# Kernel tuning notes

Hardware: AMD Instinct MI355X
Metric: run time of the kernel (lower is better)

## Reference

```python
import jax, jax.numpy as jnp
import numpy as np

T, SEQ, IN, H, L, NC = 64, 128, 256, 512, 2, 10


def _xavier(key, shape):
    fan_out, fan_in = shape[0], shape[1]
    a = jnp.sqrt(6.0 / (fan_in + fan_out)).astype(jnp.float32)
    return jax.random.uniform(key, shape, jnp.float32, -a, a)


def setup_inputs() -> dict:
    key = jax.random.key(0)
    ks = jax.random.split(key, 16)
    inp = {"x": jax.random.normal(ks[0], (T, SEQ, IN), jnp.float32)}
    # LSTM layer 0 (input IN), layer 1 (input H). PyTorch gate order: i, f, g, o
    inp["w_ih0"] = _xavier(ks[1], (4 * H, IN))
    inp["w_hh0"] = _xavier(ks[2], (4 * H, H))
    inp["b_ih0"] = jnp.zeros((4 * H,), jnp.float32)
    inp["b_hh0"] = jnp.zeros((4 * H,), jnp.float32)
    inp["w_ih1"] = _xavier(ks[3], (4 * H, H))
    inp["w_hh1"] = _xavier(ks[4], (4 * H, H))
    inp["b_ih1"] = jnp.zeros((4 * H,), jnp.float32)
    inp["b_hh1"] = jnp.zeros((4 * H,), jnp.float32)
    # out_linear: Linear(SEQ*H, H) -> ReLU -> Linear(H, NC)
    inp["w1"] = _xavier(ks[5], (H, SEQ * H))
    inp["b1"] = jnp.zeros((H,), jnp.float32)
    inp["w2"] = _xavier(ks[6], (NC, H))
    inp["b2"] = jnp.zeros((NC,), jnp.float32)
    return inp


def _lstm_layer(x, w_ih, w_hh, b_ih, b_hh):
    # x: [T, B, I]; returns hidden sequence [T, B, H]
    B = x.shape[1]
    Hh = w_hh.shape[1]
    # precompute input-to-gate contributions for all timesteps
    xg = jnp.einsum('tbi,gi->tbg', x, w_ih) + b_ih  # [T, B, 4H]

    def step(carry, xg_t):
        h, c = carry
        g = xg_t + h @ w_hh.T + b_hh  # [B, 4H]
        i, f, gg, o = jnp.split(g, 4, axis=-1)
        i = jax.nn.sigmoid(i)
        f = jax.nn.sigmoid(f)
        gg = jnp.tanh(gg)
        o = jax.nn.sigmoid(o)
        c = f * c + i * gg
        h = o * jnp.tanh(c)
        return (h, c), h

    init = (jnp.zeros((B, Hh), x.dtype), jnp.zeros((B, Hh), x.dtype))
    _, ys = jax.lax.scan(step, init, xg)
    return ys


def reference(x, w_ih0, w_hh0, b_ih0, b_hh0, w_ih1, w_hh1, b_ih1, b_hh1, w1, b1, w2, b2):
    out = _lstm_layer(x, w_ih0, w_hh0, b_ih0, b_hh0)
    out = _lstm_layer(out, w_ih1, w_hh1, b_ih1, b_hh1)  # [T, SEQ, H]
    # dropout p=0.0 -> identity
    flat = out.reshape(out.shape[0], -1)  # [T, SEQ*H] (batched version of per-i loop)
    hmid = jax.nn.relu(flat @ w1.T + b1)
    return hmid @ w2.T + b2  # [T, NC]
```

## Files before the change

### kernel.cpp

```cpp
#include <hip/hip_runtime.h>

#define TT 64
#define BB 128
#define IND 256
#define HH 512
#define GG 2048
#define NCC 10
#define KFLAT 65536
#define HP2 520
#define SP 36

typedef __attribute__((ext_vector_type(8))) short bf16x8;
typedef __attribute__((ext_vector_type(4))) float floatx4;

__device__ __forceinline__ unsigned short f2bf(float x) {
    unsigned u = __builtin_bit_cast(unsigned, x);
    u += 0x7fffu + ((u >> 16) & 1u);
    return (unsigned short)(u >> 16);
}
__device__ __forceinline__ float bf2f(unsigned short h) {
    unsigned u = ((unsigned)h) << 16;
    return __builtin_bit_cast(float, u);
}
__device__ __forceinline__ float pk2f(unsigned u) {
    float hi = __builtin_bit_cast(float, u & 0xffff0000u);
    float lo = __builtin_bit_cast(float, u << 16);
    return hi + lo;
}

__global__ __launch_bounds__(256) void pack_split_kernel(
    const float* __restrict__ src, unsigned* __restrict__ dst, int n)
{
    for (int i = blockIdx.x * 256 + threadIdx.x; i < n; i += gridDim.x * 256) {
        float f = src[i];
        unsigned short hb = f2bf(f);
        unsigned short lb = f2bf(f - bf2f(hb));
        dst[i] = ((unsigned)hb << 16) | lb;
    }
}

__global__ __launch_bounds__(256) void gemm_pk_mfma(
    const unsigned* __restrict__ A, const unsigned* __restrict__ W,
    const float* __restrict__ b0, const float* __restrict__ b1,
    float* __restrict__ C, int K, int N)
{
    __shared__ short Ahi[128][SP], Alo[128][SP], Whi[128][SP], Wlo[128][SP];

    const int tid  = threadIdx.x;
    const int lane = tid & 63;
    const int wv   = tid >> 6;
    const int wm   = (wv & 1) * 64;
    const int wn   = (wv >> 1) * 64;
    const int l15  = lane & 15;
    const int quad = lane >> 4;
    const int m0   = blockIdx.x * 128;
    const int n0   = blockIdx.y * 128;

    floatx4 acc[4][4];
    #pragma unroll
    for (int i = 0; i < 4; ++i)
        #pragma unroll
        for (int j = 0; j < 4; ++j)
            acc[i][j] = (floatx4){0.f, 0.f, 0.f, 0.f};

    for (int kc = 0; kc < K; kc += 32) {
        #pragma unroll
        for (int it = 0; it < 4; ++it) {
            const int lin = it * 256 + tid;
            const int row = lin >> 3;
            const int c4  = (lin & 7) * 4;
            uint4 va = *(const uint4*)&A[(size_t)(m0 + row) * K + kc + c4];
            uint2 ah, al;
            ah.x = (va.x >> 16) | (va.y & 0xffff0000u);
            ah.y = (va.z >> 16) | (va.w & 0xffff0000u);
            al.x = (va.x & 0xffffu) | (va.y << 16);
            al.y = (va.z & 0xffffu) | (va.w << 16);
            *(uint2*)&Ahi[row][c4] = ah;
            *(uint2*)&Alo[row][c4] = al;
            uint4 vw = *(const uint4*)&W[(size_t)(n0 + row) * K + kc + c4];
            uint2 wh, wl;
            wh.x = (vw.x >> 16) | (vw.y & 0xffff0000u);
            wh.y = (vw.z >> 16) | (vw.w & 0xffff0000u);
            wl.x = (vw.x & 0xffffu) | (vw.y << 16);
            wl.y = (vw.z & 0xffffu) | (vw.w << 16);
            *(uint2*)&Whi[row][c4] = wh;
            *(uint2*)&Wlo[row][c4] = wl;
        }
        __syncthreads();

        bf16x8 afh[4], afl[4], bfh[4], bfl[4];
        #pragma unroll
        for (int i = 0; i < 4; ++i) {
            afh[i] = *(const bf16x8*)&Ahi[wm + i * 16 + l15][quad * 8];
            afl[i] = *(const bf16x8*)&Alo[wm + i * 16 + l15][quad * 8];
            bfh[i] = *(const bf16x8*)&Whi[wn + i * 16 + l15][quad * 8];
            bfl[i] = *(const bf16x8*)&Wlo[wn + i * 16 + l15][quad * 8];
        }
        #pragma unroll
        for (int i = 0; i < 4; ++i)
            #pragma unroll
            for (int j = 0; j < 4; ++j) {
                acc[i][j] = __builtin_amdgcn_mfma_f32_16x16x32_bf16(afh[i], bfh[j], acc[i][j], 0, 0, 0);
                acc[i][j] = __builtin_amdgcn_mfma_f32_16x16x32_bf16(afh[i], bfl[j], acc[i][j], 0, 0, 0);
                acc[i][j] = __builtin_amdgcn_mfma_f32_16x16x32_bf16(afl[i], bfh[j], acc[i][j], 0, 0, 0);
            }
        __syncthreads();
    }

    #pragma unroll
    for (int i = 0; i < 4; ++i) {
        #pragma unroll
        for (int j = 0; j < 4; ++j) {
            const int n = n0 + wn + j * 16 + l15;
            const float bias = b0[n] + b1[n];
            #pragma unroll
            for (int r = 0; r < 4; ++r) {
                const int m = m0 + wm + i * 16 + quad * 4 + r;
                C[(size_t)m * N + n] = acc[i][j][r] + bias;
            }
        }
    }
}

__device__ __forceinline__ unsigned stage8_atomic(
    const unsigned long long* __restrict__ src, int bb, int kk, unsigned exp,
    short (*Hs_hi)[HP2], short (*Hs_lo)[HP2])
{
    unsigned long long q0 = __hip_atomic_load(src + 0, __ATOMIC_RELAXED, __HIP_MEMORY_SCOPE_AGENT);
    unsigned long long q1 = __hip_atomic_load(src + 1, __ATOMIC_RELAXED, __HIP_MEMORY_SCOPE_AGENT);
    unsigned long long q2 = __hip_atomic_load(src + 2, __ATOMIC_RELAXED, __HIP_MEMORY_SCOPE_AGENT);
    unsigned long long q3 = __hip_atomic_load(src + 3, __ATOMIC_RELAXED, __HIP_MEMORY_SCOPE_AGENT);
    unsigned c0 = (unsigned)q0, c1 = (unsigned)(q0 >> 32);
    unsigned c2 = (unsigned)q1, c3 = (unsigned)(q1 >> 32);
    unsigned c4 = (unsigned)q2, c5 = (unsigned)(q2 >> 32);
    unsigned c6 = (unsigned)q3, c7 = (unsigned)(q3 >> 32);
    unsigned bad = ((c0 ^ exp) | (c1 ^ exp) | (c2 ^ exp) | (c3 ^ exp)
                  | (c4 ^ exp) | (c5 ^ exp) | (c6 ^ exp) | (c7 ^ exp)) & 0xFu;
    uint4 hiv, lov;
    hiv.x = (c0 >> 16) | (c1 & 0xffff0000u);
    hiv.y = (c2 >> 16) | (c3 & 0xffff0000u);
    hiv.z = (c4 >> 16) | (c5 & 0xffff0000u);
    hiv.w = (c6 >> 16) | (c7 & 0xffff0000u);
    lov.x = (c0 & 0xFFF0u) | ((c1 & 0xFFF0u) << 16);
    lov.y = (c2 & 0xFFF0u) | ((c3 & 0xFFF0u) << 16);
    lov.z = (c4 & 0xFFF0u) | ((c5 & 0xFFF0u) << 16);
    lov.w = (c6 & 0xFFF0u) | ((c7 & 0xFFF0u) << 16);
    *(uint4*)&Hs_hi[bb][kk] = hiv;
    *(uint4*)&Hs_lo[bb][kk] = lov;
    return bad;
}

__device__ __forceinline__ unsigned stage8_plain(
    const unsigned* __restrict__ src, int bb, int kk, unsigned exp,
    short (*Hs_hi)[HP2], short (*Hs_lo)[HP2])
{
    const uint4 v0 = *(const uint4*)(src);
    const uint4 v1 = *(const uint4*)(src + 4);
    unsigned bad = ((v0.x ^ exp) | (v0.y ^ exp) | (v0.z ^ exp) | (v0.w ^ exp)
                  | (v1.x ^ exp) | (v1.y ^ exp) | (v1.z ^ exp) | (v1.w ^ exp)) & 0xFu;
    uint4 hiv, lov;
    hiv.x = (v0.x >> 16) | (v0.y & 0xffff0000u);
    hiv.y = (v0.z >> 16) | (v0.w & 0xffff0000u);
    hiv.z = (v1.x >> 16) | (v1.y & 0xffff0000u);
    hiv.w = (v1.z >> 16) | (v1.w & 0xffff0000u);
    lov.x = (v0.x & 0xFFF0u) | ((v0.y & 0xFFF0u) << 16);
    lov.y = (v0.z & 0xFFF0u) | ((v0.w & 0xFFF0u) << 16);
    lov.z = (v1.x & 0xFFF0u) | ((v1.y & 0xFFF0u) << 16);
    lov.w = (v1.z & 0xFFF0u) | ((v1.w & 0xFFF0u) << 16);
    *(uint4*)&Hs_hi[bb][kk] = hiv;
    *(uint4*)&Hs_lo[bb][kk] = lov;
    return bad;
}

__device__ __forceinline__ void stage_tile_g(
    const unsigned* __restrict__ base, unsigned exp,
    int tstart, int pcount, int pstride,
    short (*Hs_hi)[HP2], short (*Hs_lo)[HP2])
{
    unsigned miss = 0;
    for (int p = 0; p < pcount; ++p) {
        const int idx = p * pstride + tstart;
        unsigned bad = stage8_plain(base + idx, idx >> 9, idx & 511,
                                    exp, Hs_hi, Hs_lo);
        miss |= (bad ? 1u : 0u) << p;
    }
    while (miss) {
        for (int p = 0; p < pcount; ++p) {
            if (miss & (1u << p)) {
                const int idx = p * pstride + tstart;
                if (!stage8_atomic((const unsigned long long*)(base + idx),
                                   idx >> 9, idx & 511, exp, Hs_hi, Hs_lo))
                    miss &= ~(1u << p);
            }
        }
    }
}

__device__ __forceinline__ void spin_flag(const unsigned* p) {
    int n = 0;
    while (__hip_atomic_load(p, __ATOMIC_RELAXED, __HIP_MEMORY_SCOPE_AGENT) == 0u) {
        if (++n > 65536) break;
    }
}

__global__ __launch_bounds__(512, 2) void lstm_fused(
    const float* __restrict__ xg,
    const float* __restrict__ w_hh0,
    const float* __restrict__ w_ih1,
    const float* __restrict__ w_hh1,
    const float* __restrict__ b_ih1, const float* __restrict__ b_hh1,
    unsigned* __restrict__ hpack0,
    unsigned* __restrict__ hpack1,
    unsigned* __restrict__ flags)
{
    __shared__ short Ra_hi[32][HP2], Ra_lo[32][HP2];
    __shared__ short Xa_hi[32][HP2], Xa_lo[32][HP2];
    __shared__ float GsR[64][33];
    __shared__ float GsX[64][33];

    const int tid  = threadIdx.x;
    const int lane = tid & 63;
    const int wv   = tid >> 6;
    const bool isR = wv < 4;
    const int gate = wv & 3;
    const bool isB = blockIdx.x >= 128;
    const int blk  = blockIdx.x & 127;
    const int bt   = blk & 3;
    const int jsl  = blk >> 2;
    const int j0   = jsl * 16;
    const int l15  = lane & 15;
    const int quad = lane >> 4;
    const int tid_x = tid - 256;

    bf16x8 wf_hi[16], wf_lo[16];
    {
        const float* wsrc = isR ? (isB ? w_hh1 : w_hh0) : w_ih1;
        if (isR || isB) {
            const float* wrow = wsrc + (size_t)(gate * HH + j0 + l15) * HH + quad * 8;
            #pragma unroll
            for (int kc = 0; kc < 16; ++kc) {
                float f[8];
                *(float4*)&f[0] = *(const float4*)&wrow[kc * 32];
                *(float4*)&f[4] = *(const float4*)&wrow[kc * 32 + 4];
                bf16x8 vh, vl;
                #pragma unroll
                for (int j = 0; j < 8; ++j) {
                    unsigned short hb = f2bf(f[j]);
                    vh[j] = (short)hb;
                    vl[j] = (short)f2bf(f[j] - bf2f(hb));
                }
                wf_hi[kc] = vh; wf_lo[kc] = vl;
            }
        }
    }

    const int j_u = tid & 15;
    const int bu  = (tid >> 4) & 15;
    float bias_i = 0.f, bias_f = 0.f, bias_g = 0.f, bias_o = 0.f;
    if (isB && isR) {
        bias_i = b_ih1[j0 + j_u]            + b_hh1[j0 + j_u];
        bias_f = b_ih1[HH + j0 + j_u]       + b_hh1[HH + j0 + j_u];
        bias_g = b_ih1[2 * HH + j0 + j_u]   + b_hh1[2 * HH + j0 + j_u];
        bias_o = b_ih1[3 * HH + j0 + j_u]   + b_hh1[3 * HH + j0 + j_u];
    }

    for (int i = tid; i < 64 * 33; i += 512)
        ((float*)GsX)[i] = 0.f;
    __syncthreads();

    unsigned* hp_rec = isB ? hpack1 : hpack0;
    const int layerBase = isB ? 65 : 0;
    float c0 = 0.f, c1 = 0.f;

    for (int t = 0; t < TT; ++t) {
        const unsigned* rec_base = hp_rec + (size_t)t * (BB * HH) + (size_t)bt * 32 * HH;
        const unsigned* inp_base = hpack0 + (size_t)(t + 1) * (BB * HH) + (size_t)bt * 32 * HH;
        const unsigned expR = (unsigned)t % 9u;
        const unsigned expX = (unsigned)(t + 1) % 9u;
        const unsigned* fR = flags + ((layerBase + t) * 4 + bt) * 32;
        const unsigned* fX = flags + ((t + 1) * 4 + bt) * 32;

        float xgv[2][4];
        if (!isB && isR) {
            #pragma unroll
            for (int ccell = 0; ccell < 2; ++ccell) {
                const int b = bu + ccell * 16;
                const float* base = xg + (size_t)t * (BB * GG)
                                  + (size_t)(bt * 32 + b) * GG + j0 + j_u;
                xgv[ccell][0] = base[0];
                xgv[ccell][1] = base[HH];
                xgv[ccell][2] = base[2 * HH];
                xgv[ccell][3] = base[3 * HH];
            }
        }

        if (wv == 0 && lane < 32 && t > 0 && lane != jsl) spin_flag(fR + lane);
        if (isB && wv == 4 && lane < 32) spin_flag(fX + lane);
        __syncthreads();

        if (isB) {
            if (isR) stage_tile_g(rec_base, expR, tid * 8,   8, 2048, Ra_hi, Ra_lo);
            else     stage_tile_g(inp_base, expX, tid_x * 8, 8, 2048, Xa_hi, Xa_lo);
        } else {
            stage_tile_g(rec_base, expR, tid * 8, 4, 4096, Ra_hi, Ra_lo);
        }
        __syncthreads();

        if (isR) {
            floatx4 a0 = {0.f,0.f,0.f,0.f}, a1 = {0.f,0.f,0.f,0.f};
            #pragma unroll
            for (int kc = 0; kc < 16; ++kc) {
                const int off = kc * 32 + quad * 8;
                bf16x8 r0h = *(const bf16x8*)&Ra_hi[l15][off];
                bf16x8 r0l = *(const bf16x8*)&Ra_lo[l15][off];
                bf16x8 r1h = *(const bf16x8*)&Ra_hi[16 + l15][off];
                bf16x8 r1l = *(const bf16x8*)&Ra_lo[16 + l15][off];
                a0 = __builtin_amdgcn_mfma_f32_16x16x32_bf16(wf_hi[kc], r0h, a0, 0, 0, 0);
                a1 = __builtin_amdgcn_mfma_f32_16x16x32_bf16(wf_hi[kc], r1h, a1, 0, 0, 0);
                a0 = __builtin_amdgcn_mfma_f32_16x16x32_bf16(wf_hi[kc], r0l, a0, 0, 0, 0);
                a1 = __builtin_amdgcn_mfma_f32_16x16x32_bf16(wf_hi[kc], r1l, a1, 0, 0, 0);
                a0 = __builtin_amdgcn_mfma_f32_16x16x32_bf16(wf_lo[kc], r0h, a0, 0, 0, 0);
                a1 = __builtin_amdgcn_mfma_f32_16x16x32_bf16(wf_lo[kc], r1h, a1, 0, 0, 0);
            }
            #pragma unroll
            for (int r = 0; r < 4; ++r) {
                GsR[gate * 16 + quad * 4 + r][l15]      = a0[r];
                GsR[gate * 16 + quad * 4 + r][16 + l15] = a1[r];
            }
        } else if (isB) {
            floatx4 a0 = {0.f,0.f,0.f,0.f}, a1 = {0.f,0.f,0.f,0.f};
            #pragma unroll
            for (int kc = 0; kc < 16; ++kc) {
                const int off = kc * 32 + quad * 8;
                bf16x8 x0h = *(const bf16x8*)&Xa_hi[l15][off];
                bf16x8 x0l = *(const bf16x8*)&Xa_lo[l15][off];
                bf16x8 x1h = *(const bf16x8*)&Xa_hi[16 + l15][off];
                bf16x8 x1l = *(const bf16x8*)&Xa_lo[16 + l15][off];
                a0 = __builtin_amdgcn_mfma_f32_16x16x32_bf16(wf_hi[kc], x0h, a0, 0, 0, 0);
                a1 = __builtin_amdgcn_mfma_f32_16x16x32_bf16(wf_hi[kc], x1h, a1, 0, 0, 0);
                a0 = __builtin_amdgcn_mfma_f32_16x16x32_bf16(wf_hi[kc], x0l, a0, 0, 0, 0);
                a1 = __builtin_amdgcn_mfma_f32_16x16x32_bf16(wf_hi[kc], x1l, a1, 0, 0, 0);
                a0 = __builtin_amdgcn_mfma_f32_16x16x32_bf16(wf_lo[kc], x0h, a0, 0, 0, 0);
                a1 = __builtin_amdgcn_mfma_f32_16x16x32_bf16(wf_lo[kc], x1h, a1, 0, 0, 0);
            }
            #pragma unroll
            for (int r = 0; r < 4; ++r) {
                GsX[gate * 16 + quad * 4 + r][l15]      = a0[r];
                GsX[gate * 16 + quad * 4 + r][16 + l15] = a1[r];
            }
        }
        __syncthreads();

        if (isR) {
            const unsigned tag = (unsigned)(t + 1) % 9u;
            #pragma unroll
            for (int ccell = 0; ccell < 2; ++ccell) {
                const int b = bu + ccell * 16;
                float gi = GsR[j_u][b]      + GsX[j_u][b];
                float gf = GsR[16 + j_u][b] + GsX[16 + j_u][b];
                float gg = GsR[32 + j_u][b] + GsX[32 + j_u][b];
                float go = GsR[48 + j_u][b] + GsX[48 + j_u][b];
                if (isB) { gi += bias_i; gf += bias_f; gg += bias_g; go += bias_o; }
                else     { gi += xgv[ccell][0]; gf += xgv[ccell][1];
                           gg += xgv[ccell][2]; go += xgv[ccell][3]; }
                const float si = 1.f / (1.f + __expf(-gi));
                const float sf = 1.f / (1.f + __expf(-gf));
                const float tg = 2.f / (1.f + __expf(-2.f * gg)) - 1.f;
                const float so = 1.f / (1.f + __expf(-go));
                float& cr = ccell ? c1 : c0;
                cr = sf * cr + si * tg;
                const float th = 2.f / (1.f + __expf(-2.f * cr)) - 1.f;
                const float hval = so * th;
                const unsigned short hb = f2bf(hval);
                const unsigned short lb = f2bf(hval - bf2f(hb));
                const unsigned pk = ((unsigned)hb << 16) | ((unsigned)lb & 0xFFF0u) | tag;
                __hip_atomic_store(
                    &hp_rec[(size_t)(t + 1) * (BB * HH) + (size_t)(bt * 32 + b) * HH + j0 + j_u],
                    pk, __ATOMIC_RELAXED, __HIP_MEMORY_SCOPE_AGENT);
            }
        }
        __syncthreads();

        if (tid == 0)
            __hip_atomic_store(
                flags + ((layerBase + (t + 1)) * 4 + bt) * 32 + jsl,
                1u, __ATOMIC_RELAXED, __HIP_MEMORY_SCOPE_AGENT);
    }
}

__global__ __launch_bounds__(256) void cls_partial_kernel(
    const unsigned* __restrict__ A, const float* __restrict__ W,
    float* __restrict__ part)
{
    const int n0 = blockIdx.x * 64;
    const int s  = blockIdx.y;
    const int kbase = s * 2048;
    const int tid = threadIdx.x;
    __shared__ float As[32][68];
    __shared__ float Bs[32][68];
    const int tm = tid >> 4, tn = tid & 15;
    float acc[4][4] = {};

    for (int kt = 0; kt < 2048; kt += 32) {
        #pragma unroll
        for (int q = tid; q < 512; q += 256) {
            const int mm = q >> 3;
            const int kq = q & 7;
            uint4 v = *(const uint4*)&A[(size_t)mm * KFLAT + kbase + kt + kq * 4];
            As[kq*4+0][mm] = pk2f(v.x & 0xFFFFFFF0u); As[kq*4+1][mm] = pk2f(v.y & 0xFFFFFFF0u);
            As[kq*4+2][mm] = pk2f(v.z & 0xFFFFFFF0u); As[kq*4+3][mm] = pk2f(v.w & 0xFFFFFFF0u);
            float4 w = *(const float4*)&W[(size_t)(n0 + mm) * KFLAT + kbase + kt + kq * 4];
            Bs[kq*4+0][mm] = w.x; Bs[kq*4+1][mm] = w.y;
            Bs[kq*4+2][mm] = w.z; Bs[kq*4+3][mm] = w.w;
        }
        __syncthreads();
        #pragma unroll
        for (int k = 0; k < 32; ++k) {
            float4 a = *(const float4*)&As[k][tm * 4];
            float4 b = *(const float4*)&Bs[k][tn * 4];
            acc[0][0] += a.x*b.x; acc[0][1] += a.x*b.y; acc[0][2] += a.x*b.z; acc[0][3] += a.x*b.w;
            acc[1][0] += a.y*b.x; acc[1][1] += a.y*b.y; acc[1][2] += a.y*b.z; acc[1][3] += a.y*b.w;
            acc[2][0] += a.z*b.x; acc[2][1] += a.z*b.y; acc[2][2] += a.z*b.z; acc[2][3] += a.z*b.w;
            acc[3][0] += a.w*b.x; acc[3][1] += a.w*b.y; acc[3][2] += a.w*b.z; acc[3][3] += a.w*b.w;
        }
        __syncthreads();
    }
    #pragma unroll
    for (int i = 0; i < 4; ++i) {
        const int m = tm * 4 + i;
        #pragma unroll
        for (int j = 0; j < 4; ++j) {
            part[((size_t)s * 64 + m) * 512 + n0 + tn * 4 + j] = acc[i][j];
        }
    }
}

__global__ __launch_bounds__(256) void cls_final_kernel(
    const float* __restrict__ part, const float* __restrict__ b1,
    const float* __restrict__ w2, const float* __restrict__ b2,
    float* __restrict__ out)
{
    const int t = blockIdx.x;
    __shared__ float hm[512];
    for (int n = threadIdx.x; n < 512; n += 256) {
        float sacc = b1[n];
        for (int sl = 0; sl < 32; ++sl)
            sacc += part[((size_t)sl * 64 + t) * 512 + n];
        hm[n] = fmaxf(sacc, 0.f);
    }
    __syncthreads();
    if (threadIdx.x < NCC) {
        float sacc = b2[threadIdx.x];
        const float* wr = w2 + (size_t)threadIdx.x * 512;
        for (int n = 0; n < 512; ++n) sacc += hm[n] * wr[n];
        out[t * NCC + threadIdx.x] = sacc;
    }
}

extern "C" void kernel_launch(void* const* d_in, const int* in_sizes, int n_in,
                              void* d_out, int out_size, void* d_ws, size_t ws_size,
                              hipStream_t stream)
{
    const float* x     = (const float*)d_in[0];
    const float* w_ih0 = (const float*)d_in[1];
    const float* w_hh0 = (const float*)d_in[2];
    const float* b_ih0 = (const float*)d_in[3];
    const float* b_hh0 = (const float*)d_in[4];
    const float* w_ih1 = (const float*)d_in[5];
    const float* w_hh1 = (const float*)d_in[6];
    const float* b_ih1 = (const float*)d_in[7];
    const float* b_hh1 = (const float*)d_in[8];
    const float* w1    = (const float*)d_in[9];
    const float* b1    = (const float*)d_in[10];
    const float* w2    = (const float*)d_in[11];
    const float* b2    = (const float*)d_in[12];
    float* out = (float*)d_out;

    float*    ws     = (float*)d_ws;
    float*    xg     = ws;
    unsigned* hpack0 = (unsigned*)(xg + (size_t)8192 * 2048);
    unsigned* hpack1 = hpack0 + (size_t)65 * BB * HH;
    unsigned* xpk    = hpack1;
    unsigned* w0pk   = xpk + (size_t)8192 * IND;
    float*    part   = (float*)(hpack1 + (size_t)65 * BB * HH);
    unsigned* flags  = (unsigned*)part;

    pack_split_kernel<<<1024, 256, 0, stream>>>(x, xpk, 8192 * IND);
    pack_split_kernel<<<512,  256, 0, stream>>>(w_ih0, w0pk, GG * IND);
    hipMemsetAsync(hpack0, 0, (size_t)BB * HH * sizeof(unsigned), stream);
    hipMemsetAsync(flags, 0, (size_t)2 * 65 * 4 * 32 * sizeof(unsigned), stream);

    gemm_pk_mfma<<<dim3(8192 / 128, GG / 128), 256, 0, stream>>>(
        xpk, w0pk, b_ih0, b_hh0, xg, IND, GG);

    hipMemsetAsync(hpack1, 0, (size_t)BB * HH * sizeof(unsigned), stream);

    lstm_fused<<<256, 512, 0, stream>>>(
        xg, w_hh0, w_ih1, w_hh1, b_ih1, b_hh1, hpack0, hpack1, flags);

    cls_partial_kernel<<<dim3(512 / 64, 32), 256, 0, stream>>>(
        hpack1 + (size_t)BB * HH, w1, part);
    cls_final_kernel<<<64, 256, 0, stream>>>(part, b1, w2, b2, out);
}
```

Before: 818.5 us.

## Replace flag barriers with per-wave counters and distributed spin-waits in fused LSTM

Each of the four gate waves now does its own fetch-add on the per-block flag after its hidden-state stores drain, replacing the block-wide barrier plus a single flag write from thread 0. Consumers spin per lane until the counter reaches four, with s_sleep backoff, and two block-wide __syncthreads per timestep are removed. The epilogue is remapped so each thread handles two adjacent hidden units for one batch row, using float2 loads for xg and 64-bit packed atomic stores. The aim is to cut barrier latency on the recurrent critical path. In exchange, the lighter ordering between the counters and the LDS staging may be fragile, and a correctness risk remains if counters are not reset between launches.

```diff
diff --git a/kernel.cpp b/kernel.cpp
--- a/kernel.cpp
+++ b/kernel.cpp
@@ -196,9 +196,10 @@
     }
 }
 
-__device__ __forceinline__ void spin_flag(const unsigned* p) {
+__device__ __forceinline__ void spin_cnt(const unsigned* p) {
     int n = 0;
-    while (__hip_atomic_load(p, __ATOMIC_RELAXED, __HIP_MEMORY_SCOPE_AGENT) == 0u) {
+    while (__hip_atomic_load(p, __ATOMIC_RELAXED, __HIP_MEMORY_SCOPE_AGENT) < 4u) {
+        __builtin_amdgcn_s_sleep(1);
         if (++n > 65536) break;
     }
 }
@@ -231,6 +232,7 @@
     const int l15  = lane & 15;
     const int quad = lane >> 4;
     const int tid_x = tid - 256;
+    const int slice = (lane >> 1);
 
     bf16x8 wf_hi[16], wf_lo[16];
     {
@@ -254,14 +256,18 @@
         }
     }
 
-    const int j_u = tid & 15;
-    const int bu  = (tid >> 4) & 15;
-    float bias_i = 0.f, bias_f = 0.f, bias_g = 0.f, bias_o = 0.f;
+    const int ju  = (tid & 7) * 2;
+    const int bu2 = (tid >> 3) & 31;
+    float bi0=0.f,bi1=0.f,bf0_=0.f,bf1_=0.f,bg0=0.f,bg1=0.f,bo0=0.f,bo1=0.f;
     if (isB && isR) {
-        bias_i = b_ih1[j0 + j_u]            + b_hh1[j0 + j_u];
-        bias_f = b_ih1[HH + j0 + j_u]       + b_hh1[HH + j0 + j_u];
-        bias_g = b_ih1[2 * HH + j0 + j_u]   + b_hh1[2 * HH + j0 + j_u];
-        bias_o = b_ih1[3 * HH + j0 + j_u]   + b_hh1[3 * HH + j0 + j_u];
+        bi0 = b_ih1[j0+ju]        + b_hh1[j0+ju];
+        bi1 = b_ih1[j0+ju+1]      + b_hh1[j0+ju+1];
+        bf0_= b_ih1[HH+j0+ju]     + b_hh1[HH+j0+ju];
+        bf1_= b_ih1[HH+j0+ju+1]   + b_hh1[HH+j0+ju+1];
+        bg0 = b_ih1[2*HH+j0+ju]   + b_hh1[2*HH+j0+ju];
+        bg1 = b_ih1[2*HH+j0+ju+1] + b_hh1[2*HH+j0+ju+1];
+        bo0 = b_ih1[3*HH+j0+ju]   + b_hh1[3*HH+j0+ju];
+        bo1 = b_ih1[3*HH+j0+ju+1] + b_hh1[3*HH+j0+ju+1];
     }
 
     for (int i = tid; i < 64 * 33; i += 512)
@@ -277,26 +283,25 @@
         const unsigned* inp_base = hpack0 + (size_t)(t + 1) * (BB * HH) + (size_t)bt * 32 * HH;
         const unsigned expR = (unsigned)t % 9u;
         const unsigned expX = (unsigned)(t + 1) % 9u;
-        const unsigned* fR = flags + ((layerBase + t) * 4 + bt) * 32;
-        const unsigned* fX = flags + ((t + 1) * 4 + bt) * 32;
-
-        float xgv[2][4];
+        const unsigned* cR = flags + ((layerBase + t) * 4 + bt) * 32;
+        const unsigned* cX = flags + ((t + 1) * 4 + bt) * 32;
+
+        float2 xgv[4];
         if (!isB && isR) {
-            #pragma unroll
-            for (int ccell = 0; ccell < 2; ++ccell) {
-                const int b = bu + ccell * 16;
-                const float* base = xg + (size_t)t * (BB * GG)
-                                  + (size_t)(bt * 32 + b) * GG + j0 + j_u;
-                xgv[ccell][0] = base[0];
-                xgv[ccell][1] = base[HH];
-                xgv[ccell][2] = base[2 * HH];
-                xgv[ccell][3] = base[3 * HH];
-            }
-        }
-
-        if (wv == 0 && lane < 32 && t > 0 && lane != jsl) spin_flag(fR + lane);
-        if (isB && wv == 4 && lane < 32) spin_flag(fX + lane);
-        __syncthreads();
+            const float* base = xg + (size_t)t * (BB * GG)
+                              + (size_t)(bt * 32 + bu2) * GG + j0 + ju;
+            #pragma unroll
+            for (int g = 0; g < 4; ++g)
+                xgv[g] = *(const float2*)&base[g * HH];
+        }
+
+        if (isB) {
+            if (isR) { if (t > 0) spin_cnt(cR + slice); }
+            else     { spin_cnt(cX + slice); }
+        } else {
+            if (t > 0) spin_cnt(cR + slice);
+        }
+        asm volatile("" ::: "memory");
 
         if (isB) {
             if (isR) stage_tile_g(rec_base, expR, tid * 8,   8, 2048, Ra_hi, Ra_lo);
@@ -353,38 +358,56 @@
 
         if (isR) {
             const unsigned tag = (unsigned)(t + 1) % 9u;
-            #pragma unroll
-            for (int ccell = 0; ccell < 2; ++ccell) {
-                const int b = bu + ccell * 16;
-                float gi = GsR[j_u][b]      + GsX[j_u][b];
-                float gf = GsR[16 + j_u][b] + GsX[16 + j_u][b];
-                float gg = GsR[32 + j_u][b] + GsX[32 + j_u][b];
-                float go = GsR[48 + j_u][b] + GsX[48 + j_u][b];
-                if (isB) { gi += bias_i; gf += bias_f; gg += bias_g; go += bias_o; }
-                else     { gi += xgv[ccell][0]; gf += xgv[ccell][1];
-                           gg += xgv[ccell][2]; go += xgv[ccell][3]; }
-                const float si = 1.f / (1.f + __expf(-gi));
-                const float sf = 1.f / (1.f + __expf(-gf));
-                const float tg = 2.f / (1.f + __expf(-2.f * gg)) - 1.f;
-                const float so = 1.f / (1.f + __expf(-go));
-                float& cr = ccell ? c1 : c0;
-                cr = sf * cr + si * tg;
-                const float th = 2.f / (1.f + __expf(-2.f * cr)) - 1.f;
-                const float hval = so * th;
-                const unsigned short hb = f2bf(hval);
-                const unsigned short lb = f2bf(hval - bf2f(hb));
-                const unsigned pk = ((unsigned)hb << 16) | ((unsigned)lb & 0xFFF0u) | tag;
-                __hip_atomic_store(
-                    &hp_rec[(size_t)(t + 1) * (BB * HH) + (size_t)(bt * 32 + b) * HH + j0 + j_u],
-                    pk, __ATOMIC_RELAXED, __HIP_MEMORY_SCOPE_AGENT);
-            }
-        }
-        __syncthreads();
-
-        if (tid == 0)
+            float gi0 = GsR[ju][bu2]      + GsX[ju][bu2];
+            float gi1 = GsR[ju+1][bu2]    + GsX[ju+1][bu2];
+            float gf0 = GsR[16+ju][bu2]   + GsX[16+ju][bu2];
+            float gf1 = GsR[17+ju][bu2]   + GsX[17+ju][bu2];
+            float gg0 = GsR[32+ju][bu2]   + GsX[32+ju][bu2];
+            float gg1 = GsR[33+ju][bu2]   + GsX[33+ju][bu2];
+            float go0 = GsR[48+ju][bu2]   + GsX[48+ju][bu2];
+            float go1 = GsR[49+ju][bu2]   + GsX[49+ju][bu2];
+            if (isB) {
+                gi0 += bi0; gi1 += bi1; gf0 += bf0_; gf1 += bf1_;
+                gg0 += bg0; gg1 += bg1; go0 += bo0; go1 += bo1;
+            } else {
+                gi0 += xgv[0].x; gi1 += xgv[0].y;
+                gf0 += xgv[1].x; gf1 += xgv[1].y;
+                gg0 += xgv[2].x; gg1 += xgv[2].y;
+                go0 += xgv[3].x; go1 += xgv[3].y;
+            }
+            const float si0 = 1.f / (1.f + __expf(-gi0));
+            const float sf0 = 1.f / (1.f + __expf(-gf0));
+            const float tg0 = 2.f / (1.f + __expf(-2.f * gg0)) - 1.f;
+            const float so0 = 1.f / (1.f + __expf(-go0));
+            c0 = sf0 * c0 + si0 * tg0;
+            const float th0 = 2.f / (1.f + __expf(-2.f * c0)) - 1.f;
+            const float h0v = so0 * th0;
+            const float si1 = 1.f / (1.f + __expf(-gi1));
+            const float sf1 = 1.f / (1.f + __expf(-gf1));
+            const float tg1 = 2.f / (1.f + __expf(-2.f * gg1)) - 1.f;
+            const float so1 = 1.f / (1.f + __expf(-go1));
+            c1 = sf1 * c1 + si1 * tg1;
+            const float th1 = 2.f / (1.f + __expf(-2.f * c1)) - 1.f;
+            const float h1v = so1 * th1;
+            const unsigned short hb0 = f2bf(h0v);
+            const unsigned short lb0 = f2bf(h0v - bf2f(hb0));
+            const unsigned short hb1 = f2bf(h1v);
+            const unsigned short lb1 = f2bf(h1v - bf2f(hb1));
+            const unsigned pk0 = ((unsigned)hb0 << 16) | ((unsigned)lb0 & 0xFFF0u) | tag;
+            const unsigned pk1 = ((unsigned)hb1 << 16) | ((unsigned)lb1 & 0xFFF0u) | tag;
+            const unsigned long long pk64 =
+                (unsigned long long)pk0 | ((unsigned long long)pk1 << 32);
             __hip_atomic_store(
-                flags + ((layerBase + (t + 1)) * 4 + bt) * 32 + jsl,
-                1u, __ATOMIC_RELAXED, __HIP_MEMORY_SCOPE_AGENT);
+                (unsigned long long*)&hp_rec[(size_t)(t + 1) * (BB * HH)
+                    + (size_t)(bt * 32 + bu2) * HH + j0 + ju],
+                pk64, __ATOMIC_RELAXED, __HIP_MEMORY_SCOPE_AGENT);
+
+            asm volatile("s_waitcnt vmcnt(0)" ::: "memory");
+            if (lane == 0)
+                __hip_atomic_fetch_add(
+                    (unsigned*)(flags + ((layerBase + (t + 1)) * 4 + bt) * 32 + jsl),
+                    1u, __ATOMIC_RELAXED, __HIP_MEMORY_SCOPE_AGENT);
+        }
     }
 }
 
```

Result: slower. 1.193 ms (+45.8%).

## Fuse layer-0 input projection into persistent LSTM kernel, drop xg GEMM

Applied to the files above, without the earlier changes.

Removes the separate pack kernels and the large input-projection GEMM that wrote a 64x128x2048 fp32 xg buffer. Layer-0 blocks now use their previously idle X-waves to load w_ih0 fragments into registers once, convert x[t] to split bf16 in LDS each step, and compute the input gate contributions with MFMA alongside the recurrent part. This cuts a kernel launch and the xg write and re-read. In exchange, the per-step critical path of layer 0 gains the x conversion and an extra MFMA loop, and layer-0 R-waves now stage the full tile rather than half.

```diff
diff --git a/kernel.cpp b/kernel.cpp
--- a/kernel.cpp
+++ b/kernel.cpp
@@ -8,7 +8,6 @@
 #define NCC 10
 #define KFLAT 65536
 #define HP2 520
-#define SP 36
 
 typedef __attribute__((ext_vector_type(8))) short bf16x8;
 typedef __attribute__((ext_vector_type(4))) float floatx4;
@@ -26,100 +25,6 @@
     float hi = __builtin_bit_cast(float, u & 0xffff0000u);
     float lo = __builtin_bit_cast(float, u << 16);
     return hi + lo;
-}
-
-__global__ __launch_bounds__(256) void pack_split_kernel(
-    const float* __restrict__ src, unsigned* __restrict__ dst, int n)
-{
-    for (int i = blockIdx.x * 256 + threadIdx.x; i < n; i += gridDim.x * 256) {
-        float f = src[i];
-        unsigned short hb = f2bf(f);
-        unsigned short lb = f2bf(f - bf2f(hb));
-        dst[i] = ((unsigned)hb << 16) | lb;
-    }
-}
-
-__global__ __launch_bounds__(256) void gemm_pk_mfma(
-    const unsigned* __restrict__ A, const unsigned* __restrict__ W,
-    const float* __restrict__ b0, const float* __restrict__ b1,
-    float* __restrict__ C, int K, int N)
-{
-    __shared__ short Ahi[128][SP], Alo[128][SP], Whi[128][SP], Wlo[128][SP];
-
-    const int tid  = threadIdx.x;
-    const int lane = tid & 63;
-    const int wv   = tid >> 6;
-    const int wm   = (wv & 1) * 64;
-    const int wn   = (wv >> 1) * 64;
-    const int l15  = lane & 15;
-    const int quad = lane >> 4;
-    const int m0   = blockIdx.x * 128;
-    const int n0   = blockIdx.y * 128;
-
-    floatx4 acc[4][4];
-    #pragma unroll
-    for (int i = 0; i < 4; ++i)
-        #pragma unroll
-        for (int j = 0; j < 4; ++j)
-            acc[i][j] = (floatx4){0.f, 0.f, 0.f, 0.f};
-
-    for (int kc = 0; kc < K; kc += 32) {
-        #pragma unroll
-        for (int it = 0; it < 4; ++it) {
-            const int lin = it * 256 + tid;
-            const int row = lin >> 3;
-            const int c4  = (lin & 7) * 4;
-            uint4 va = *(const uint4*)&A[(size_t)(m0 + row) * K + kc + c4];
-            uint2 ah, al;
-            ah.x = (va.x >> 16) | (va.y & 0xffff0000u);
-            ah.y = (va.z >> 16) | (va.w & 0xffff0000u);
-            al.x = (va.x & 0xffffu) | (va.y << 16);
-            al.y = (va.z & 0xffffu) | (va.w << 16);
-            *(uint2*)&Ahi[row][c4] = ah;
-            *(uint2*)&Alo[row][c4] = al;
-            uint4 vw = *(const uint4*)&W[(size_t)(n0 + row) * K + kc + c4];
-            uint2 wh, wl;
-            wh.x = (vw.x >> 16) | (vw.y & 0xffff0000u);
-            wh.y = (vw.z >> 16) | (vw.w & 0xffff0000u);
-            wl.x = (vw.x & 0xffffu) | (vw.y << 16);
-            wl.y = (vw.z & 0xffffu) | (vw.w << 16);
-            *(uint2*)&Whi[row][c4] = wh;
-            *(uint2*)&Wlo[row][c4] = wl;
-        }
-        __syncthreads();
-
-        bf16x8 afh[4], afl[4], bfh[4], bfl[4];
-        #pragma unroll
-        for (int i = 0; i < 4; ++i) {
-            afh[i] = *(const bf16x8*)&Ahi[wm + i * 16 + l15][quad * 8];
-            afl[i] = *(const bf16x8*)&Alo[wm + i * 16 + l15][quad * 8];
-            bfh[i] = *(const bf16x8*)&Whi[wn + i * 16 + l15][quad * 8];
-            bfl[i] = *(const bf16x8*)&Wlo[wn + i * 16 + l15][quad * 8];
-        }
-        #pragma unroll
-        for (int i = 0; i < 4; ++i)
-            #pragma unroll
-            for (int j = 0; j < 4; ++j) {
-                acc[i][j] = __builtin_amdgcn_mfma_f32_16x16x32_bf16(afh[i], bfh[j], acc[i][j], 0, 0, 0);
-                acc[i][j] = __builtin_amdgcn_mfma_f32_16x16x32_bf16(afh[i], bfl[j], acc[i][j], 0, 0, 0);
-                acc[i][j] = __builtin_amdgcn_mfma_f32_16x16x32_bf16(afl[i], bfh[j], acc[i][j], 0, 0, 0);
-            }
-        __syncthreads();
-    }
-
-    #pragma unroll
-    for (int i = 0; i < 4; ++i) {
-        #pragma unroll
-        for (int j = 0; j < 4; ++j) {
-            const int n = n0 + wn + j * 16 + l15;
-            const float bias = b0[n] + b1[n];
-            #pragma unroll
-            for (int r = 0; r < 4; ++r) {
-                const int m = m0 + wm + i * 16 + quad * 4 + r;
-                C[(size_t)m * N + n] = acc[i][j][r] + bias;
-            }
-        }
-    }
 }
 
 __device__ __forceinline__ unsigned stage8_atomic(
@@ -204,10 +109,12 @@
 }
 
 __global__ __launch_bounds__(512, 2) void lstm_fused(
-    const float* __restrict__ xg,
+    const float* __restrict__ x,
     const float* __restrict__ w_hh0,
+    const float* __restrict__ w_ih0,
     const float* __restrict__ w_ih1,
     const float* __restrict__ w_hh1,
+    const float* __restrict__ b_ih0, const float* __restrict__ b_hh0,
     const float* __restrict__ b_ih1, const float* __restrict__ b_hh1,
     unsigned* __restrict__ hpack0,
     unsigned* __restrict__ hpack1,
@@ -234,39 +141,38 @@
 
     bf16x8 wf_hi[16], wf_lo[16];
     {
-        const float* wsrc = isR ? (isB ? w_hh1 : w_hh0) : w_ih1;
-        if (isR || isB) {
-            const float* wrow = wsrc + (size_t)(gate * HH + j0 + l15) * HH + quad * 8;
-            #pragma unroll
-            for (int kc = 0; kc < 16; ++kc) {
-                float f[8];
-                *(float4*)&f[0] = *(const float4*)&wrow[kc * 32];
-                *(float4*)&f[4] = *(const float4*)&wrow[kc * 32 + 4];
-                bf16x8 vh, vl;
-                #pragma unroll
-                for (int j = 0; j < 8; ++j) {
-                    unsigned short hb = f2bf(f[j]);
-                    vh[j] = (short)hb;
-                    vl[j] = (short)f2bf(f[j] - bf2f(hb));
-                }
-                wf_hi[kc] = vh; wf_lo[kc] = vl;
-            }
+        const float* wsrc;
+        int kstride, nfrag;
+        if (isR)      { wsrc = isB ? w_hh1 : w_hh0; kstride = HH;  nfrag = 16; }
+        else if (isB) { wsrc = w_ih1;               kstride = HH;  nfrag = 16; }
+        else          { wsrc = w_ih0;               kstride = IND; nfrag = 8;  }
+        const float* wrow = wsrc + (size_t)(gate * HH + j0 + l15) * kstride + quad * 8;
+        for (int kc = 0; kc < nfrag; ++kc) {
+            float f[8];
+            *(float4*)&f[0] = *(const float4*)&wrow[kc * 32];
+            *(float4*)&f[4] = *(const float4*)&wrow[kc * 32 + 4];
+            bf16x8 vh, vl;
+            #pragma unroll
+            for (int j = 0; j < 8; ++j) {
+                unsigned short hb = f2bf(f[j]);
+                vh[j] = (short)hb;
+                vl[j] = (short)f2bf(f[j] - bf2f(hb));
+            }
+            wf_hi[kc] = vh; wf_lo[kc] = vl;
         }
     }
 
     const int j_u = tid & 15;
     const int bu  = (tid >> 4) & 15;
     float bias_i = 0.f, bias_f = 0.f, bias_g = 0.f, bias_o = 0.f;
-    if (isB && isR) {
-        bias_i = b_ih1[j0 + j_u]            + b_hh1[j0 + j_u];
-        bias_f = b_ih1[HH + j0 + j_u]       + b_hh1[HH + j0 + j_u];
-        bias_g = b_ih1[2 * HH + j0 + j_u]   + b_hh1[2 * HH + j0 + j_u];
-        bias_o = b_ih1[3 * HH + j0 + j_u]   + b_hh1[3 * HH + j0 + j_u];
-    }
-
-    for (int i = tid; i < 64 * 33; i += 512)
-        ((float*)GsX)[i] = 0.f;
-    __syncthreads();
+    if (isR) {
+        const float* bA = isB ? b_ih1 : b_ih0;
+        const float* bB = isB ? b_hh1 : b_hh0;
+        bias_i = bA[j0 + j_u]            + bB[j0 + j_u];
+        bias_f = bA[HH + j0 + j_u]       + bB[HH + j0 + j_u];
+        bias_g = bA[2 * HH + j0 + j_u]   + bB[2 * HH + j0 + j_u];
+        bias_o = bA[3 * HH + j0 + j_u]   + bB[3 * HH + j0 + j_u];
+    }
 
     unsigned* hp_rec = isB ? hpack1 : hpack0;
     const int layerBase = isB ? 65 : 0;
@@ -280,29 +186,34 @@
         const unsigned* fR = flags + ((layerBase + t) * 4 + bt) * 32;
         const unsigned* fX = flags + ((t + 1) * 4 + bt) * 32;
 
-        float xgv[2][4];
-        if (!isB && isR) {
-            #pragma unroll
-            for (int ccell = 0; ccell < 2; ++ccell) {
-                const int b = bu + ccell * 16;
-                const float* base = xg + (size_t)t * (BB * GG)
-                                  + (size_t)(bt * 32 + b) * GG + j0 + j_u;
-                xgv[ccell][0] = base[0];
-                xgv[ccell][1] = base[HH];
-                xgv[ccell][2] = base[2 * HH];
-                xgv[ccell][3] = base[3 * HH];
-            }
-        }
-
         if (wv == 0 && lane < 32 && t > 0 && lane != jsl) spin_flag(fR + lane);
         if (isB && wv == 4 && lane < 32) spin_flag(fX + lane);
         __syncthreads();
 
-        if (isB) {
-            if (isR) stage_tile_g(rec_base, expR, tid * 8,   8, 2048, Ra_hi, Ra_lo);
-            else     stage_tile_g(inp_base, expX, tid_x * 8, 8, 2048, Xa_hi, Xa_lo);
+        if (isR) {
+            stage_tile_g(rec_base, expR, tid * 8, 8, 2048, Ra_hi, Ra_lo);
+        } else if (isB) {
+            stage_tile_g(inp_base, expX, tid_x * 8, 8, 2048, Xa_hi, Xa_lo);
         } else {
-            stage_tile_g(rec_base, expR, tid * 8, 4, 4096, Ra_hi, Ra_lo);
+            const int row = tid_x >> 3;
+            const int cb  = (tid_x & 7) * 32;
+            const float* src = x + (size_t)t * (BB * IND)
+                             + (size_t)(bt * 32 + row) * IND + cb;
+            #pragma unroll
+            for (int q = 0; q < 4; ++q) {
+                float f[8];
+                *(float4*)&f[0] = *(const float4*)&src[q * 8];
+                *(float4*)&f[4] = *(const float4*)&src[q * 8 + 4];
+                short hs[8], ls[8];
+                #pragma unroll
+                for (int j = 0; j < 8; ++j) {
+                    unsigned short hb = f2bf(f[j]);
+                    hs[j] = (short)hb;
+                    ls[j] = (short)f2bf(f[j] - bf2f(hb));
+                }
+                *(uint4*)&Xa_hi[row][cb + q * 8] = *(const uint4*)hs;
+                *(uint4*)&Xa_lo[row][cb + q * 8] = *(const uint4*)ls;
+            }
         }
         __syncthreads();
 
@@ -327,10 +238,10 @@
                 GsR[gate * 16 + quad * 4 + r][l15]      = a0[r];
                 GsR[gate * 16 + quad * 4 + r][16 + l15] = a1[r];
             }
-        } else if (isB) {
+        } else {
+            const int nkc = isB ? 16 : 8;
             floatx4 a0 = {0.f,0.f,0.f,0.f}, a1 = {0.f,0.f,0.f,0.f};
-            #pragma unroll
-            for (int kc = 0; kc < 16; ++kc) {
+            for (int kc = 0; kc < nkc; ++kc) {
                 const int off = kc * 32 + quad * 8;
                 bf16x8 x0h = *(const bf16x8*)&Xa_hi[l15][off];
                 bf16x8 x0l = *(const bf16x8*)&Xa_lo[l15][off];
@@ -356,13 +267,10 @@
             #pragma unroll
             for (int ccell = 0; ccell < 2; ++ccell) {
                 const int b = bu + ccell * 16;
-                float gi = GsR[j_u][b]      + GsX[j_u][b];
-                float gf = GsR[16 + j_u][b] + GsX[16 + j_u][b];
-                float gg = GsR[32 + j_u][b] + GsX[32 + j_u][b];
-                float go = GsR[48 + j_u][b] + GsX[48 + j_u][b];
-                if (isB) { gi += bias_i; gf += bias_f; gg += bias_g; go += bias_o; }
-                else     { gi += xgv[ccell][0]; gf += xgv[ccell][1];
-                           gg += xgv[ccell][2]; go += xgv[ccell][3]; }
+                float gi = GsR[j_u][b]      + GsX[j_u][b]      + bias_i;
+                float gf = GsR[16 + j_u][b] + GsX[16 + j_u][b] + bias_f;
+                float gg = GsR[32 + j_u][b] + GsX[32 + j_u][b] + bias_g;
+                float go = GsR[48 + j_u][b] + GsX[48 + j_u][b] + bias_o;
                 const float si = 1.f / (1.f + __expf(-gi));
                 const float sf = 1.f / (1.f + __expf(-gf));
                 const float tg = 2.f / (1.f + __expf(-2.f * gg)) - 1.f;
@@ -476,27 +384,18 @@
     const float* b2    = (const float*)d_in[12];
     float* out = (float*)d_out;
 
-    float*    ws     = (float*)d_ws;
-    float*    xg     = ws;
-    unsigned* hpack0 = (unsigned*)(xg + (size_t)8192 * 2048);
+    unsigned* hpack0 = (unsigned*)d_ws;
     unsigned* hpack1 = hpack0 + (size_t)65 * BB * HH;
-    unsigned* xpk    = hpack1;
-    unsigned* w0pk   = xpk + (size_t)8192 * IND;
     float*    part   = (float*)(hpack1 + (size_t)65 * BB * HH);
     unsigned* flags  = (unsigned*)part;
 
-    pack_split_kernel<<<1024, 256, 0, stream>>>(x, xpk, 8192 * IND);
-    pack_split_kernel<<<512,  256, 0, stream>>>(w_ih0, w0pk, GG * IND);
     hipMemsetAsync(hpack0, 0, (size_t)BB * HH * sizeof(unsigned), stream);
+    hipMemsetAsync(hpack1, 0, (size_t)BB * HH * sizeof(unsigned), stream);
     hipMemsetAsync(flags, 0, (size_t)2 * 65 * 4 * 32 * sizeof(unsigned), stream);
 
-    gemm_pk_mfma<<<dim3(8192 / 128, GG / 128), 256, 0, stream>>>(
-        xpk, w0pk, b_ih0, b_hh0, xg, IND, GG);
-
-    hipMemsetAsync(hpack1, 0, (size_t)BB * HH * sizeof(unsigned), stream);
-
     lstm_fused<<<256, 512, 0, stream>>>(
-        xg, w_hh0, w_ih1, w_hh1, b_ih1, b_hh1, hpack0, hpack1, flags);
+        x, w_hh0, w_ih0, w_ih1, w_hh1, b_ih0, b_hh0, b_ih1, b_hh1,
+        hpack0, hpack1, flags);
 
     cls_partial_kernel<<<dim3(512 / 64, 32), 256, 0, stream>>>(
         hpack1 + (size_t)BB * HH, w1, part);
```

After: 1.412 ms. +72.5%, slower.
